# Kernel optimization log

Hardware: AMD Instinct MI355X
Metric: run time of the kernel (lower is better)

Reference implementation:

```python
import jax, jax.numpy as jnp
import numpy as np

B, S, DIM = 2, 2048, 2048
H, KVH, HD = 16, 4, 128
G = H // KVH  # GQA groups = 4
THETA = 10000.0


def setup_inputs() -> dict:
    key = jax.random.key(0)
    k0, k1, k2, k3, k4 = jax.random.split(key, 5)
    x = jax.random.normal(k0, (B, S, DIM), jnp.float32)
    # RoPE table: [max_seq_len, head_dim//2, 2] holding (cos, sin)
    inv_freq = 1.0 / (THETA ** (jnp.arange(0, HD, 2, dtype=jnp.float32) / HD))
    angles = jnp.outer(jnp.arange(S, dtype=jnp.float32), inv_freq)  # [S, HD//2]
    freqs_cis = jnp.stack([jnp.cos(angles), jnp.sin(angles)], axis=-1)
    sc = 0.02
    wq = jax.random.normal(k1, (H * HD, DIM), jnp.float32) * sc
    wk = jax.random.normal(k2, (KVH * HD, DIM), jnp.float32) * sc
    wv = jax.random.normal(k3, (KVH * HD, DIM), jnp.float32) * sc
    wo = jax.random.normal(k4, (DIM, H * HD), jnp.float32) * sc
    return {"x": x, "freqs_cis": freqs_cis, "wq": wq, "wk": wk, "wv": wv, "wo": wo}


def apply_rope(x, freqs_cis):
    # x: [B, S, h, HD]; freqs_cis: [max_S, HD//2, 2]
    s = x.shape[1]
    xr = x.astype(jnp.float32).reshape(*x.shape[:-1], -1, 2)  # [B,S,h,HD//2,2]
    cos = freqs_cis[:s, :, 0][None, :, None, :]  # [1,S,1,HD//2]
    sin = freqs_cis[:s, :, 1][None, :, None, :]
    x0, x1 = xr[..., 0], xr[..., 1]
    out = jnp.stack([x0 * cos - x1 * sin, x0 * sin + x1 * cos], axis=-1)
    return out.reshape(x.shape).astype(x.dtype)


def reference(x, freqs_cis, wq, wk, wv, wo):
    b, s, d = x.shape
    q = (x @ wq.T).reshape(b, s, H, HD)
    k = (x @ wk.T).reshape(b, s, KVH, HD)
    v = (x @ wv.T).reshape(b, s, KVH, HD)
    q = apply_rope(q, freqs_cis)
    k = apply_rope(k, freqs_cis)
    # GQA expand: repeat_interleave along head dim
    k = jnp.repeat(k, G, axis=2)  # [b,s,H,HD]
    v = jnp.repeat(v, G, axis=2)
    q = jnp.swapaxes(q, 1, 2)  # [b,H,s,HD]
    k = jnp.swapaxes(k, 1, 2)
    v = jnp.swapaxes(v, 1, 2)
    scale = 1.0 / jnp.sqrt(jnp.asarray(HD, dtype=q.dtype))
    scores = jnp.einsum('bhqd,bhkd->bhqk', q, k) * scale  # [b,H,s,s]
    causal = jnp.tril(jnp.ones((s, s), dtype=bool))
    scores = jnp.where(causal[None, None], scores, jnp.finfo(scores.dtype).min)
    probs = jax.nn.softmax(scores, axis=-1)
    attn = jnp.einsum('bhqk,bhkd->bhqd', probs, v)  # [b,H,s,HD]
    attn = jnp.swapaxes(attn, 1, 2).reshape(b, s, H * HD)
    return attn @ wo.T
```

## Files before the change

kernel.cpp:

```cpp
#include <hip/hip_runtime.h>
#include <stdint.h>

#define B_ 2
#define S_ 2048
#define DIM_ 2048
#define H_ 16
#define KVH_ 4
#define HD_ 128

typedef short short8 __attribute__((ext_vector_type(8)));
typedef float f4 __attribute__((ext_vector_type(4)));
typedef unsigned short u16;

#define KSCALE (0.08838834764831845f * 1.4426950408889634f)

__device__ __forceinline__ float bf2f(u16 u) {
    union { unsigned int i; float f; } c; c.i = ((unsigned int)u) << 16; return c.f;
}
__device__ __forceinline__ u16 f2bf(float f) {
    union { float f; unsigned int i; } c; c.f = f;
    return (u16)((c.i + 0x7fffu + ((c.i >> 16) & 1u)) >> 16);
}

#define GLDS16(gp, lp) \
    __builtin_amdgcn_global_load_lds((const __attribute__((address_space(1))) unsigned int*)(gp), \
                                     (__attribute__((address_space(3))) unsigned int*)(lp), 16, 0, 0)

__global__ void cast_all(const float* __restrict__ x,  const float* __restrict__ wq,
                         const float* __restrict__ wk, const float* __restrict__ wv,
                         const float* __restrict__ wo,
                         u16* __restrict__ xb, u16* __restrict__ wqkvb, u16* __restrict__ wob) {
    int i = blockIdx.x * 256 + threadIdx.x;
    const float4* src; ushort4* dst; int j;
    if (i < 2097152)      { src = (const float4*)x;  dst = (ushort4*)xb;                 j = i; }
    else if (i < 3145728) { src = (const float4*)wq; dst = (ushort4*)wqkvb;              j = i - 2097152; }
    else if (i < 3407872) { src = (const float4*)wk; dst = (ushort4*)wqkvb + 1048576;    j = i - 3145728; }
    else if (i < 3670016) { src = (const float4*)wv; dst = (ushort4*)wqkvb + 1310720;    j = i - 3407872; }
    else                  { src = (const float4*)wo; dst = (ushort4*)wob;                j = i - 3670016; }
    float4 v = src[j];
    ushort4 o;
    o.x = f2bf(v.x); o.y = f2bf(v.y); o.z = f2bf(v.z); o.w = f2bf(v.w);
    dst[j] = o;
}

template<bool OUT_BF16, int NBX>
__global__ __launch_bounds__(256) void gemm_bt(const u16* __restrict__ A,
                                               const u16* __restrict__ W,
                                               void* __restrict__ Cout,
                                               int M, int N, int K) {
    __shared__ u16 As[128 * 32];
    __shared__ u16 Bs[128 * 32];
    int t = threadIdx.x, lane = t & 63, w = t >> 6;
    int quad = lane >> 4, l16 = lane & 15;
    int wm = w & 1, wn = w >> 1;
    int bid = blockIdx.x;
    int xcd = bid & 7, grp = bid >> 3;
    int bx = grp % NBX, by = (grp / NBX) * 8 + xcd;
    size_t m0 = (size_t)by * 128, n0 = (size_t)bx * 128;

    int c0 = w * 2;
    int ar = c0 * 16 + (lane >> 2);
    int ac = (lane & 3) * 8;
    const u16* Abase = A + (m0 + ar) * (size_t)K + ac;
    const u16* Bbase = W + (n0 + ar) * (size_t)K + ac;
    u16* Adst = As + c0 * 512;
    u16* Bdst = Bs + c0 * 512;

    f4 acc[4][4];
    #pragma unroll
    for (int i = 0; i < 4; i++)
        #pragma unroll
        for (int j = 0; j < 4; j++) acc[i][j] = (f4){0.f, 0.f, 0.f, 0.f};

    int nk = K >> 5;
    for (int kt = 0; kt < nk; kt++) {
        const u16* ga = Abase + kt * 32;
        const u16* gb = Bbase + kt * 32;
        GLDS16(ga, Adst);
        GLDS16(ga + 16 * (size_t)K, Adst + 512);
        GLDS16(gb, Bdst);
        GLDS16(gb + 16 * (size_t)K, Bdst + 512);
        __syncthreads();
        short8 a[4], b[4];
        #pragma unroll
        for (int i = 0; i < 4; i++) a[i] = *(const short8*)&As[(wm * 64 + i * 16 + l16) * 32 + quad * 8];
        #pragma unroll
        for (int j = 0; j < 4; j++) b[j] = *(const short8*)&Bs[(wn * 64 + j * 16 + l16) * 32 + quad * 8];
        #pragma unroll
        for (int i = 0; i < 4; i++)
            #pragma unroll
            for (int j = 0; j < 4; j++)
                acc[i][j] = __builtin_amdgcn_mfma_f32_16x16x32_bf16(a[i], b[j], acc[i][j], 0, 0, 0);
        __syncthreads();
    }
    #pragma unroll
    for (int i = 0; i < 4; i++) {
        size_t row = m0 + wm * 64 + i * 16 + quad * 4;
        #pragma unroll
        for (int j = 0; j < 4; j++) {
            size_t col = n0 + wn * 64 + j * 16 + l16;
            #pragma unroll
            for (int r = 0; r < 4; r++) {
                if (OUT_BF16) ((u16*)Cout)[(row + r) * N + col] = f2bf(acc[i][j][r]);
                else          ((float*)Cout)[(row + r) * N + col] = acc[i][j][r];
            }
        }
    }
}

__global__ __launch_bounds__(256) void pack_k(const u16* __restrict__ QKV,
                                              const float* __restrict__ freqs,
                                              u16* __restrict__ Kp) {
    int gid = blockIdx.x * 256 + threadIdx.x;
    int lane = gid & 63;
    int fid = (gid >> 6) & 15;
    int kt = (gid >> 10) & 31;
    int bk = gid >> 15;
    int b = bk >> 2, kvh = bk & 3;
    int n = fid >> 2, c = fid & 3;
    int l16 = lane & 15, quad = lane >> 4;
    int s = kt * 64 + n * 16 + l16;
    const u16* src = QKV + (size_t)(b * 2048 + s) * 3072 + 2048 + kvh * 128 + c * 32 + quad * 8;
    short8 v = *(const short8*)src;
    short8 o;
    #pragma unroll
    for (int jp = 0; jp < 4; jp++) {
        int hd2 = c * 16 + quad * 4 + jp;
        float2 cw = ((const float2*)freqs)[s * 64 + hd2];
        float x0 = bf2f((u16)v[2 * jp]), x1 = bf2f((u16)v[2 * jp + 1]);
        o[2 * jp]     = (short)f2bf(x0 * cw.x - x1 * cw.y);
        o[2 * jp + 1] = (short)f2bf(x0 * cw.y + x1 * cw.x);
    }
    *(short8*)&Kp[(size_t)gid * 8] = o;
}

__global__ __launch_bounds__(256) void pack_v(const u16* __restrict__ QKV, u16* __restrict__ Vp) {
    __shared__ u16 L[64 * 136];
    int bid = blockIdx.x;
    int bk = bid & 7, kt = bid >> 3;
    int b = bk >> 2, kvh = bk & 3;
    int t = threadIdx.x;
    const u16* src = QKV + (size_t)(b * 2048 + kt * 64) * 3072 + 2560 + kvh * 128;
    #pragma unroll
    for (int it = 0; it < 4; it++) {
        int idx = t + it * 256;
        int r = idx >> 4, c = idx & 15;
        *(short8*)&L[r * 136 + c * 8] = *(const short8*)(src + (size_t)r * 3072 + c * 8);
    }
    __syncthreads();
    u16* dst = Vp + ((size_t)bk * 32 + kt) * 8192;
    #pragma unroll
    for (int it = 0; it < 4; it++) {
        int idx = t + it * 256;
        int fid = idx >> 6, lane = idx & 63;
        int nt = fid >> 1, kc = fid & 1;
        int l16 = lane & 15, quad = lane >> 4;
        int hd = nt * 16 + l16;
        int s0 = kc * 32 + quad * 8;
        short8 v;
        #pragma unroll
        for (int j = 0; j < 8; j++) v[j] = (short)L[(s0 + j) * 136 + hd];
        *(short8*)&dst[(size_t)idx * 8] = v;
    }
}

__global__ __launch_bounds__(256) __attribute__((amdgpu_waves_per_eu(2, 2)))
void attn_kernel(const u16* __restrict__ QKV,
                 const float* __restrict__ freqs,
                 const u16* __restrict__ Kp,
                 const u16* __restrict__ Vp,
                 u16* __restrict__ Ob) {
    __shared__ u16 Ks[2][8192];
    __shared__ u16 Vs[2][8192];
    __shared__ u16 Ps[4 * 1024];
    int bid = blockIdx.x;
    int bk = bid & 7, pr = bid >> 3;
    int b = bk >> 2, kvh = bk & 3;
    int t = threadIdx.x, lane = t & 63, w = t >> 6, quad = lane >> 4, l16 = lane & 15;
    int l7 = l16 & 7, hi = l16 >> 3;
    int h = kvh * 4 + w;

    short8 ones;
    #pragma unroll
    for (int j = 0; j < 8; j++) ones[j] = (short)0x3F80;

    const u16* Kpb = Kp + (size_t)bk * 32 * 8192;
    const u16* Vpb = Vp + (size_t)bk * 32 * 8192;
    u16* P = Ps + w * 1024;

    for (int ph = 0; ph < 2; ph++) {
        int qt = ph ? pr : 127 - pr;
        int nkt = (qt >> 2) + 1;

        short8 qf[4];
        {
            int s = qt * 16 + l16;
            const u16* qp = QKV + ((size_t)(b * S_ + s)) * 3072 + h * HD_ + quad * 8;
            const float2* fr2 = (const float2*)freqs;
            #pragma unroll
            for (int c = 0; c < 4; c++) {
                short8 v = *(const short8*)(qp + c * 32);
                short8 o;
                #pragma unroll
                for (int jp = 0; jp < 4; jp++) {
                    float2 cs = fr2[s * 64 + c * 16 + quad * 4 + jp];
                    float x0 = bf2f((u16)v[2 * jp]), x1 = bf2f((u16)v[2 * jp + 1]);
                    o[2 * jp]     = (short)f2bf((x0 * cs.x - x1 * cs.y) * KSCALE);
                    o[2 * jp + 1] = (short)f2bf((x0 * cs.y + x1 * cs.x) * KSCALE);
                }
                qf[c] = o;
            }
        }
        float m_i = -3e38f;
        f4 ls = (f4){0.f, 0.f, 0.f, 0.f};
        f4 o[8];
        #pragma unroll
        for (int n = 0; n < 8; n++) o[n] = (f4){0.f, 0.f, 0.f, 0.f};

        {
            const u16* ks = Kpb + (w * 4) * 512 + lane * 8;
            const u16* vs = Vpb + (w * 4) * 512 + lane * 8;
            #pragma unroll
            for (int i = 0; i < 4; i++) {
                GLDS16(ks + i * 512, &Ks[0][(w * 4 + i) * 512]);
                GLDS16(vs + i * 512, &Vs[0][(w * 4 + i) * 512]);
            }
        }

        for (int kt = 0; kt < nkt; kt++) {
            int buf = kt & 1;
            __syncthreads();
            if (kt + 1 < nkt) {
                int nb = buf ^ 1;
                const u16* ks = Kpb + (size_t)(kt + 1) * 8192 + (w * 4) * 512 + lane * 8;
                const u16* vs = Vpb + (size_t)(kt + 1) * 8192 + (w * 4) * 512 + lane * 8;
                #pragma unroll
                for (int i = 0; i < 4; i++) {
                    GLDS16(ks + i * 512, &Ks[nb][(w * 4 + i) * 512]);
                    GLDS16(vs + i * 512, &Vs[nb][(w * 4 + i) * 512]);
                }
            }

            f4 sc[4];
            #pragma unroll
            for (int n = 0; n < 4; n++) sc[n] = (f4){0.f, 0.f, 0.f, 0.f};
            #pragma unroll
            for (int n = 0; n < 4; n++) {
                #pragma unroll
                for (int c = 0; c < 4; c++) {
                    short8 kf = *(const short8*)&Ks[buf][(n * 4 + c) * 512 + lane * 8];
                    sc[n] = __builtin_amdgcn_mfma_f32_16x16x32_bf16(qf[c], kf, sc[n], 0, 0, 0);
                }
            }
            if (kt == nkt - 1) {
                int qrow0 = qt * 16 + quad * 4;
                #pragma unroll
                for (int n = 0; n < 4; n++) {
                    int colg = kt * 64 + n * 16 + l16;
                    #pragma unroll
                    for (int r = 0; r < 4; r++)
                        sc[n][r] = (colg <= qrow0 + r) ? sc[n][r] : -3e38f;
                }
            }
            float gm = fmaxf(fmaxf(sc[0][0], sc[0][1]), fmaxf(sc[0][2], sc[0][3]));
            #pragma unroll
            for (int n = 1; n < 4; n++)
                gm = fmaxf(gm, fmaxf(fmaxf(sc[n][0], sc[n][1]), fmaxf(sc[n][2], sc[n][3])));
            #pragma unroll
            for (int off = 1; off < 64; off <<= 1) gm = fmaxf(gm, __shfl_xor(gm, off, 64));
            float mnew = fmaxf(m_i, gm);
            if (mnew > m_i) {
                float al = exp2f(m_i - mnew);
                m_i = mnew;
                #pragma unroll
                for (int r = 0; r < 4; r++) ls[r] *= al;
                #pragma unroll
                for (int nt = 0; nt < 8; nt++)
                    #pragma unroll
                    for (int r = 0; r < 4; r++) o[nt][r] *= al;
            }
            #pragma unroll
            for (int n = 0; n < 4; n++) {
                #pragma unroll
                for (int r = 0; r < 4; r++) {
                    float p = exp2f(sc[n][r] - m_i);
                    union { float f; unsigned int u; } cv; cv.f = p;
                    int row = quad * 4 + r;
                    int sw = (n * 2 + hi) ^ (row & 7);
                    P[row * 64 + sw * 8 + l7] = (u16)(cv.u >> 16);
                }
            }
            __asm__ volatile("s_waitcnt lgkmcnt(0)" ::: "memory");

            #pragma unroll
            for (int kc = 0; kc < 2; kc++) {
                short8 af = *(const short8*)&P[l16 * 64 + (((kc * 4 + quad) ^ l7) << 3)];
                ls = __builtin_amdgcn_mfma_f32_16x16x32_bf16(af, ones, ls, 0, 0, 0);
                #pragma unroll
                for (int nt = 0; nt < 8; nt++) {
                    short8 vf = *(const short8*)&Vs[buf][(nt * 2 + kc) * 512 + lane * 8];
                    o[nt] = __builtin_amdgcn_mfma_f32_16x16x32_bf16(af, vf, o[nt], 0, 0, 0);
                }
            }
        }
        float rl[4];
        #pragma unroll
        for (int r = 0; r < 4; r++) rl[r] = 1.0f / ls[r];
        #pragma unroll
        for (int nt = 0; nt < 8; nt++)
            #pragma unroll
            for (int r = 0; r < 4; r++) {
                size_t row = (size_t)b * S_ + qt * 16 + quad * 4 + r;
                Ob[row * 2048 + h * HD_ + nt * 16 + l16] = f2bf(o[nt][r] * rl[r]);
            }
        __syncthreads();
    }
}

extern "C" void kernel_launch(void* const* d_in, const int* in_sizes, int n_in,
                              void* d_out, int out_size, void* d_ws, size_t ws_size,
                              hipStream_t stream) {
    const float* x     = (const float*)d_in[0];
    const float* freqs = (const float*)d_in[1];
    const float* wq    = (const float*)d_in[2];
    const float* wk    = (const float*)d_in[3];
    const float* wv    = (const float*)d_in[4];
    const float* wo    = (const float*)d_in[5];
    float* out = (float*)d_out;

    char* p = (char*)d_ws;
    u16* xb    = (u16*)p; p += (size_t)4096 * 2048 * 2;
    u16* wqkvb = (u16*)p; p += (size_t)3072 * 2048 * 2;
    u16* wob   = (u16*)p; p += (size_t)2048 * 2048 * 2;
    u16* QKVb  = (u16*)p; p += (size_t)4096 * 3072 * 2;
    u16* Kpb   = (u16*)p; p += (size_t)8 * 32 * 8192 * 2;
    u16* Vpb   = (u16*)p; p += (size_t)8 * 32 * 8192 * 2;
    u16* attnb = xb;

    cast_all<<<18432, 256, 0, stream>>>(x, wq, wk, wv, wo, xb, wqkvb, wob);

    gemm_bt<true, 24><<<768, 256, 0, stream>>>(xb, wqkvb, QKVb, 4096, 3072, 2048);

    pack_k<<<1024, 256, 0, stream>>>(QKVb, freqs, Kpb);
    pack_v<<<256, 256, 0, stream>>>(QKVb, Vpb);

    attn_kernel<<<512, 256, 0, stream>>>(QKVb, freqs, Kpb, Vpb, attnb);

    gemm_bt<false, 16><<<512, 256, 0, stream>>>(attnb, wob, out, 4096, 2048, 2048);
}
```

Before: 319.1 us.

## Rewrite attention with 32x32 MFMA, transposed S, register-resident P, lazy rescale

The attention kernel moves from 16x16x32 to 32x32x16 bf16 MFMAs. It computes S^T = K·Q^T so each lane owns one query column, which lets the row max use a single cross-lane shuffle instead of a full wave reduction. P is packed to bf16 in registers with v_cvt_pk_bf16_f32 and permlane32_swap and fed straight into the PV MFMA, removing the LDS round trip for P and the ones-MFMA row sum. The online-softmax rescale only fires when the max grows by more than 8, skipping most rescales. K and V packing switches to an XOR-swizzled row layout to match the new LDS reads, and blocks now take 32-row query tiles with one tile per block instead of two phases, which changes the load balance.

```diff
diff --git a/kernel.cpp b/kernel.cpp
--- a/kernel.cpp
+++ b/kernel.cpp
@@ -10,6 +10,8 @@
 
 typedef short short8 __attribute__((ext_vector_type(8)));
 typedef float f4 __attribute__((ext_vector_type(4)));
+typedef float f16v __attribute__((ext_vector_type(16)));
+typedef unsigned int uint2v __attribute__((ext_vector_type(2)));
 typedef unsigned short u16;
 
 #define KSCALE (0.08838834764831845f * 1.4426950408889634f)
@@ -20,6 +22,11 @@
 __device__ __forceinline__ u16 f2bf(float f) {
     union { float f; unsigned int i; } c; c.f = f;
     return (u16)((c.i + 0x7fffu + ((c.i >> 16) & 1u)) >> 16);
+}
+__device__ __forceinline__ unsigned pk_bf16(float lo, float hi) {
+    unsigned r;
+    asm("v_cvt_pk_bf16_f32 %0, %1, %2" : "=v"(r) : "v"(lo), "v"(hi));
+    return r;
 }
 
 #define GLDS16(gp, lp) \
@@ -112,21 +119,16 @@
                                               const float* __restrict__ freqs,
                                               u16* __restrict__ Kp) {
     int gid = blockIdx.x * 256 + threadIdx.x;
-    int lane = gid & 63;
-    int fid = (gid >> 6) & 15;
-    int kt = (gid >> 10) & 31;
-    int bk = gid >> 15;
+    int u = gid & 15, row = (gid >> 4) & 63, kt = (gid >> 10) & 31, bk = gid >> 15;
     int b = bk >> 2, kvh = bk & 3;
-    int n = fid >> 2, c = fid & 3;
-    int l16 = lane & 15, quad = lane >> 4;
-    int s = kt * 64 + n * 16 + l16;
-    const u16* src = QKV + (size_t)(b * 2048 + s) * 3072 + 2048 + kvh * 128 + c * 32 + quad * 8;
+    int s = kt * 64 + row;
+    int d8 = u ^ (row & 7);
+    const u16* src = QKV + (size_t)(b * S_ + s) * 3072 + 2048 + kvh * HD_ + d8 * 8;
     short8 v = *(const short8*)src;
     short8 o;
     #pragma unroll
     for (int jp = 0; jp < 4; jp++) {
-        int hd2 = c * 16 + quad * 4 + jp;
-        float2 cw = ((const float2*)freqs)[s * 64 + hd2];
+        float2 cw = ((const float2*)freqs)[s * 64 + d8 * 4 + jp];
         float x0 = bf2f((u16)v[2 * jp]), x1 = bf2f((u16)v[2 * jp + 1]);
         o[2 * jp]     = (short)f2bf(x0 * cw.x - x1 * cw.y);
         o[2 * jp + 1] = (short)f2bf(x0 * cw.y + x1 * cw.x);
@@ -140,7 +142,7 @@
     int bk = bid & 7, kt = bid >> 3;
     int b = bk >> 2, kvh = bk & 3;
     int t = threadIdx.x;
-    const u16* src = QKV + (size_t)(b * 2048 + kt * 64) * 3072 + 2560 + kvh * 128;
+    const u16* src = QKV + (size_t)(b * S_ + kt * 64) * 3072 + 2560 + kvh * HD_;
     #pragma unroll
     for (int it = 0; it < 4; it++) {
         int idx = t + it * 256;
@@ -148,18 +150,15 @@
         *(short8*)&L[r * 136 + c * 8] = *(const short8*)(src + (size_t)r * 3072 + c * 8);
     }
     __syncthreads();
-    u16* dst = Vp + ((size_t)bk * 32 + kt) * 8192;
+    u16* dst = Vp + (size_t)(bk * 32 + kt) * 8192;
     #pragma unroll
     for (int it = 0; it < 4; it++) {
         int idx = t + it * 256;
-        int fid = idx >> 6, lane = idx & 63;
-        int nt = fid >> 1, kc = fid & 1;
-        int l16 = lane & 15, quad = lane >> 4;
-        int hd = nt * 16 + l16;
-        int s0 = kc * 32 + quad * 8;
+        int hd = idx >> 3, u = idx & 7;
+        int k0 = (u ^ (hd & 7)) * 8;
         short8 v;
         #pragma unroll
-        for (int j = 0; j < 8; j++) v[j] = (short)L[(s0 + j) * 136 + hd];
+        for (int jj = 0; jj < 8; jj++) v[jj] = (short)L[(k0 + jj) * 136 + hd];
         *(short8*)&dst[(size_t)idx * 8] = v;
     }
 }
@@ -172,148 +171,164 @@
                  u16* __restrict__ Ob) {
     __shared__ u16 Ks[2][8192];
     __shared__ u16 Vs[2][8192];
-    __shared__ u16 Ps[4 * 1024];
     int bid = blockIdx.x;
-    int bk = bid & 7, pr = bid >> 3;
+    int jj_ = bid & 255, half = bid >> 8;
+    int bk = jj_ & 7, qpr = jj_ >> 3;
+    int qb = half ? qpr : 63 - qpr;
     int b = bk >> 2, kvh = bk & 3;
-    int t = threadIdx.x, lane = t & 63, w = t >> 6, quad = lane >> 4, l16 = lane & 15;
-    int l7 = l16 & 7, hi = l16 >> 3;
+    int t = threadIdx.x, lane = t & 63, w = t >> 6;
+    int l31 = lane & 31, hi = lane >> 5, l7 = lane & 7;
     int h = kvh * 4 + w;
-
-    short8 ones;
-    #pragma unroll
-    for (int j = 0; j < 8; j++) ones[j] = (short)0x3F80;
+    int nkt = (qb >> 1) + 1;
+
+    short8 qf[8];
+    {
+        int s = qb * 32 + l31;
+        const u16* qp = QKV + ((size_t)(b * S_ + s)) * 3072 + h * HD_ + hi * 8;
+        const float2* fr2 = (const float2*)freqs;
+        #pragma unroll
+        for (int ds = 0; ds < 8; ds++) {
+            short8 v = *(const short8*)(qp + ds * 16);
+            short8 o;
+            #pragma unroll
+            for (int jp = 0; jp < 4; jp++) {
+                float2 cs = fr2[s * 64 + ds * 8 + hi * 4 + jp];
+                float x0 = bf2f((u16)v[2 * jp]), x1 = bf2f((u16)v[2 * jp + 1]);
+                o[2 * jp]     = (short)f2bf((x0 * cs.x - x1 * cs.y) * KSCALE);
+                o[2 * jp + 1] = (short)f2bf((x0 * cs.y + x1 * cs.x) * KSCALE);
+            }
+            qf[ds] = o;
+        }
+    }
+
+    float m_i = -3e38f, ls = 0.f;
+    f16v o4[4];
+    #pragma unroll
+    for (int i = 0; i < 4; i++)
+        #pragma unroll
+        for (int r = 0; r < 16; r++) o4[i][r] = 0.f;
 
     const u16* Kpb = Kp + (size_t)bk * 32 * 8192;
     const u16* Vpb = Vp + (size_t)bk * 32 * 8192;
-    u16* P = Ps + w * 1024;
-
-    for (int ph = 0; ph < 2; ph++) {
-        int qt = ph ? pr : 127 - pr;
-        int nkt = (qt >> 2) + 1;
-
-        short8 qf[4];
-        {
-            int s = qt * 16 + l16;
-            const u16* qp = QKV + ((size_t)(b * S_ + s)) * 3072 + h * HD_ + quad * 8;
-            const float2* fr2 = (const float2*)freqs;
-            #pragma unroll
-            for (int c = 0; c < 4; c++) {
-                short8 v = *(const short8*)(qp + c * 32);
-                short8 o;
+    int so = w * 2048 + lane * 8;
+
+    {
+        const u16* ks = Kpb + so;
+        const u16* vs = Vpb + so;
+        #pragma unroll
+        for (int i = 0; i < 4; i++) {
+            GLDS16(ks + i * 512, &Ks[0][w * 2048 + i * 512]);
+            GLDS16(vs + i * 512, &Vs[0][w * 2048 + i * 512]);
+        }
+    }
+
+    for (int kt = 0; kt < nkt; kt++) {
+        int buf = kt & 1;
+        __syncthreads();
+        if (kt + 1 < nkt) {
+            int nb = buf ^ 1;
+            const u16* ks = Kpb + (size_t)(kt + 1) * 8192 + so;
+            const u16* vs = Vpb + (size_t)(kt + 1) * 8192 + so;
+            #pragma unroll
+            for (int i = 0; i < 4; i++) {
+                GLDS16(ks + i * 512, &Ks[nb][w * 2048 + i * 512]);
+                GLDS16(vs + i * 512, &Vs[nb][w * 2048 + i * 512]);
+            }
+        }
+
+        f16v sacc[2];
+        #pragma unroll
+        for (int k2 = 0; k2 < 2; k2++)
+            #pragma unroll
+            for (int r = 0; r < 16; r++) sacc[k2][r] = 0.f;
+        #pragma unroll
+        for (int ds = 0; ds < 8; ds++) {
+            int uK = ((ds * 2 + hi) ^ l7) * 8;
+            short8 kf0 = *(const short8*)&Ks[buf][l31 * 128 + uK];
+            short8 kf1 = *(const short8*)&Ks[buf][(32 + l31) * 128 + uK];
+            sacc[0] = __builtin_amdgcn_mfma_f32_32x32x16_bf16(kf0, qf[ds], sacc[0], 0, 0, 0);
+            sacc[1] = __builtin_amdgcn_mfma_f32_32x32x16_bf16(kf1, qf[ds], sacc[1], 0, 0, 0);
+        }
+
+        if (kt == nkt - 1) {
+            int off0 = kt * 64 - qb * 32;
+            #pragma unroll
+            for (int k2 = 0; k2 < 2; k2++) {
                 #pragma unroll
-                for (int jp = 0; jp < 4; jp++) {
-                    float2 cs = fr2[s * 64 + c * 16 + quad * 4 + jp];
-                    float x0 = bf2f((u16)v[2 * jp]), x1 = bf2f((u16)v[2 * jp + 1]);
-                    o[2 * jp]     = (short)f2bf((x0 * cs.x - x1 * cs.y) * KSCALE);
-                    o[2 * jp + 1] = (short)f2bf((x0 * cs.y + x1 * cs.x) * KSCALE);
+                for (int r = 0; r < 16; r++) {
+                    int colo = off0 + k2 * 32 + (r & 3) + ((r >> 2) << 3) + (hi << 2);
+                    if (colo > l31) sacc[k2][r] = -3e38f;
                 }
-                qf[c] = o;
-            }
-        }
-        float m_i = -3e38f;
-        f4 ls = (f4){0.f, 0.f, 0.f, 0.f};
-        f4 o[8];
-        #pragma unroll
-        for (int n = 0; n < 8; n++) o[n] = (f4){0.f, 0.f, 0.f, 0.f};
-
-        {
-            const u16* ks = Kpb + (w * 4) * 512 + lane * 8;
-            const u16* vs = Vpb + (w * 4) * 512 + lane * 8;
-            #pragma unroll
-            for (int i = 0; i < 4; i++) {
-                GLDS16(ks + i * 512, &Ks[0][(w * 4 + i) * 512]);
-                GLDS16(vs + i * 512, &Vs[0][(w * 4 + i) * 512]);
-            }
-        }
-
-        for (int kt = 0; kt < nkt; kt++) {
-            int buf = kt & 1;
-            __syncthreads();
-            if (kt + 1 < nkt) {
-                int nb = buf ^ 1;
-                const u16* ks = Kpb + (size_t)(kt + 1) * 8192 + (w * 4) * 512 + lane * 8;
-                const u16* vs = Vpb + (size_t)(kt + 1) * 8192 + (w * 4) * 512 + lane * 8;
+            }
+        }
+
+        float pm = sacc[0][0];
+        #pragma unroll
+        for (int r = 1; r < 16; r++) pm = fmaxf(pm, sacc[0][r]);
+        #pragma unroll
+        for (int r = 0; r < 16; r++) pm = fmaxf(pm, sacc[1][r]);
+        pm = fmaxf(pm, __shfl_xor(pm, 32, 64));
+        if (__any(pm > m_i + 8.0f)) {
+            float mnew = fmaxf(m_i, pm);
+            float al = exp2f(m_i - mnew);
+            ls *= al;
+            #pragma unroll
+            for (int i = 0; i < 4; i++)
                 #pragma unroll
-                for (int i = 0; i < 4; i++) {
-                    GLDS16(ks + i * 512, &Ks[nb][(w * 4 + i) * 512]);
-                    GLDS16(vs + i * 512, &Vs[nb][(w * 4 + i) * 512]);
-                }
-            }
-
-            f4 sc[4];
-            #pragma unroll
-            for (int n = 0; n < 4; n++) sc[n] = (f4){0.f, 0.f, 0.f, 0.f};
-            #pragma unroll
-            for (int n = 0; n < 4; n++) {
-                #pragma unroll
-                for (int c = 0; c < 4; c++) {
-                    short8 kf = *(const short8*)&Ks[buf][(n * 4 + c) * 512 + lane * 8];
-                    sc[n] = __builtin_amdgcn_mfma_f32_16x16x32_bf16(qf[c], kf, sc[n], 0, 0, 0);
-                }
-            }
-            if (kt == nkt - 1) {
-                int qrow0 = qt * 16 + quad * 4;
-                #pragma unroll
-                for (int n = 0; n < 4; n++) {
-                    int colg = kt * 64 + n * 16 + l16;
-                    #pragma unroll
-                    for (int r = 0; r < 4; r++)
-                        sc[n][r] = (colg <= qrow0 + r) ? sc[n][r] : -3e38f;
-                }
-            }
-            float gm = fmaxf(fmaxf(sc[0][0], sc[0][1]), fmaxf(sc[0][2], sc[0][3]));
-            #pragma unroll
-            for (int n = 1; n < 4; n++)
-                gm = fmaxf(gm, fmaxf(fmaxf(sc[n][0], sc[n][1]), fmaxf(sc[n][2], sc[n][3])));
-            #pragma unroll
-            for (int off = 1; off < 64; off <<= 1) gm = fmaxf(gm, __shfl_xor(gm, off, 64));
-            float mnew = fmaxf(m_i, gm);
-            if (mnew > m_i) {
-                float al = exp2f(m_i - mnew);
-                m_i = mnew;
-                #pragma unroll
-                for (int r = 0; r < 4; r++) ls[r] *= al;
-                #pragma unroll
-                for (int nt = 0; nt < 8; nt++)
-                    #pragma unroll
-                    for (int r = 0; r < 4; r++) o[nt][r] *= al;
-            }
-            #pragma unroll
-            for (int n = 0; n < 4; n++) {
-                #pragma unroll
-                for (int r = 0; r < 4; r++) {
-                    float p = exp2f(sc[n][r] - m_i);
-                    union { float f; unsigned int u; } cv; cv.f = p;
-                    int row = quad * 4 + r;
-                    int sw = (n * 2 + hi) ^ (row & 7);
-                    P[row * 64 + sw * 8 + l7] = (u16)(cv.u >> 16);
-                }
-            }
-            __asm__ volatile("s_waitcnt lgkmcnt(0)" ::: "memory");
-
-            #pragma unroll
-            for (int kc = 0; kc < 2; kc++) {
-                short8 af = *(const short8*)&P[l16 * 64 + (((kc * 4 + quad) ^ l7) << 3)];
-                ls = __builtin_amdgcn_mfma_f32_16x16x32_bf16(af, ones, ls, 0, 0, 0);
-                #pragma unroll
-                for (int nt = 0; nt < 8; nt++) {
-                    short8 vf = *(const short8*)&Vs[buf][(nt * 2 + kc) * 512 + lane * 8];
-                    o[nt] = __builtin_amdgcn_mfma_f32_16x16x32_bf16(af, vf, o[nt], 0, 0, 0);
-                }
-            }
-        }
-        float rl[4];
-        #pragma unroll
-        for (int r = 0; r < 4; r++) rl[r] = 1.0f / ls[r];
-        #pragma unroll
-        for (int nt = 0; nt < 8; nt++)
-            #pragma unroll
-            for (int r = 0; r < 4; r++) {
-                size_t row = (size_t)b * S_ + qt * 16 + quad * 4 + r;
-                Ob[row * 2048 + h * HD_ + nt * 16 + l16] = f2bf(o[nt][r] * rl[r]);
-            }
-        __syncthreads();
+                for (int r = 0; r < 16; r++) o4[i][r] *= al;
+            m_i = mnew;
+        }
+
+        short8 pa[4];
+        #pragma unroll
+        for (int k2 = 0; k2 < 2; k2++) {
+            float p[16];
+            #pragma unroll
+            for (int r = 0; r < 16; r++) {
+                p[r] = exp2f(sacc[k2][r] - m_i);
+                ls += p[r];
+            }
+            unsigned W0 = pk_bf16(p[0], p[1]),   W1 = pk_bf16(p[2], p[3]);
+            unsigned W2 = pk_bf16(p[4], p[5]),   W3 = pk_bf16(p[6], p[7]);
+            unsigned W4 = pk_bf16(p[8], p[9]),   W5 = pk_bf16(p[10], p[11]);
+            unsigned W6 = pk_bf16(p[12], p[13]), W7 = pk_bf16(p[14], p[15]);
+            uint2v r02 = __builtin_amdgcn_permlane32_swap(W0, W2, false, false);
+            uint2v r13 = __builtin_amdgcn_permlane32_swap(W1, W3, false, false);
+            uint2v r46 = __builtin_amdgcn_permlane32_swap(W4, W6, false, false);
+            uint2v r57 = __builtin_amdgcn_permlane32_swap(W5, W7, false, false);
+            union { unsigned u[4]; short8 s8; } flo, fhi;
+            flo.u[0] = r02[0]; flo.u[1] = r13[0]; flo.u[2] = r02[1]; flo.u[3] = r13[1];
+            fhi.u[0] = r46[0]; fhi.u[1] = r57[0]; fhi.u[2] = r46[1]; fhi.u[3] = r57[1];
+            pa[k2 * 2]     = flo.s8;
+            pa[k2 * 2 + 1] = fhi.s8;
+        }
+
+        #pragma unroll
+        for (int ks = 0; ks < 4; ks++) {
+            int uV = ((ks * 2 + hi) ^ l7) * 8;
+            #pragma unroll
+            for (int ht = 0; ht < 4; ht++) {
+                short8 vf = *(const short8*)&Vs[buf][(ht * 32 + l31) * 64 + uV];
+                o4[ht] = __builtin_amdgcn_mfma_f32_32x32x16_bf16(vf, pa[ks], o4[ht], 0, 0, 0);
+            }
+        }
+    }
+
+    ls += __shfl_xor(ls, 32, 64);
+    float rl = 1.0f / ls;
+    size_t row = (size_t)b * S_ + qb * 32 + l31;
+    u16* op = Ob + row * 2048 + h * HD_;
+    #pragma unroll
+    for (int ht = 0; ht < 4; ht++) {
+        #pragma unroll
+        for (int g = 0; g < 4; g++) {
+            ushort4 st;
+            st.x = f2bf(o4[ht][4 * g + 0] * rl);
+            st.y = f2bf(o4[ht][4 * g + 1] * rl);
+            st.z = f2bf(o4[ht][4 * g + 2] * rl);
+            st.w = f2bf(o4[ht][4 * g + 3] * rl);
+            *(ushort4*)&op[ht * 32 + g * 8 + hi * 4] = st;
+        }
     }
 }
 
```

New measurement: 319.9 us. Within noise of the previous version (+0.3%).
